# Kernel optimization log

Measured on AMD Instinct MI355X. Metric: run time of the kernel, lower is better.

The kernel has to match this reference:

```python
import jax, jax.numpy as jnp
import numpy as np

EMBED = 1024
HEADS = 16
HEAD_DIM = EMBED // HEADS
B, S = 2, 2048


def setup_inputs() -> dict:
    key = jax.random.key(0)
    ks = jax.random.split(key, 13)
    def lin(kw, kb):
        # torch nn.Linear default init: U(-1/sqrt(fan_in), 1/sqrt(fan_in))
        bound = 1.0 / np.sqrt(EMBED)
        W = jax.random.uniform(kw, (EMBED, EMBED), jnp.float32, -bound, bound)
        b = jax.random.uniform(kb, (EMBED,), jnp.float32, -bound, bound)
        return W, b
    Wq, bq = lin(ks[0], ks[1])
    Wk, bk = lin(ks[2], ks[3])
    Wv, bv = lin(ks[4], ks[5])
    Wo, bo = lin(ks[6], ks[7])
    return {
        "query": jax.random.normal(ks[8], (B, S, EMBED), jnp.float32),
        "key": jax.random.normal(ks[9], (B, S, EMBED), jnp.float32),
        "value": jax.random.normal(ks[10], (B, S, EMBED), jnp.float32),
        "mask": jax.random.randint(ks[11], (B, S, S), 0, 2, jnp.int32),
        "Wq": Wq, "bq": bq, "Wk": Wk, "bk": bk,
        "Wv": Wv, "bv": bv, "Wo": Wo, "bo": bo,
    }


def _split_heads(x):
    b, s, _ = x.shape
    return x.reshape(b, s, HEADS, HEAD_DIM).transpose(0, 2, 1, 3)  # [B,H,S,D]


def reference(query, key, value, mask, Wq, bq, Wk, bk, Wv, bv, Wo, bo):
    scaling = HEAD_DIM ** -0.5
    q = _split_heads(query @ Wq.T + bq) * scaling          # [B,H,Sq,D]
    k = _split_heads(key @ Wk.T + bk)                       # [B,H,Sk,D]
    v = _split_heads(value @ Wv.T + bv)                     # [B,H,Sk,D]
    scores = jnp.einsum('bhqd,bhkd->bhqk', q, k)            # [B,H,Sq,Sk]
    scores = jnp.where(mask[:, None, :, :] == 0, jnp.float32(-10000.0), scores)
    p = jax.nn.softmax(scores, axis=-1)
    x = jnp.einsum('bhqk,bhkd->bhqd', p, v)                 # [B,H,Sq,D]
    b, h, s, d = x.shape
    x = x.transpose(0, 2, 1, 3).reshape(b, s, h * d)
    return x @ Wo.T + bo
```

## Files before the change

kernel.cpp:

```cpp
#include <hip/hip_runtime.h>

#define EMBED 1024
#define HEADS 16
#define HDIM  64
#define BATCH 2
#define SEQ   2048
#define MTOT  (BATCH*SEQ)
#define LOG2E 1.4426950408889634f
#define QSCALE (0.125f * LOG2E)

typedef __attribute__((ext_vector_type(8)))  short short8;
typedef __attribute__((ext_vector_type(4)))  float f32x4;
typedef __attribute__((ext_vector_type(16))) float f32x16;

#define MFMA(a,b,c)   __builtin_amdgcn_mfma_f32_16x16x32_bf16(a,b,c,0,0,0)
#define MFMA32(a,b,c) __builtin_amdgcn_mfma_f32_32x32x16_bf16(a,b,c,0,0,0)

__device__ __forceinline__ ushort f2bf(float f) {
  union { float f; unsigned u; } v; v.f = f;
  unsigned u = v.u;
  unsigned r = u + 0x7fffu + ((u >> 16) & 1u);
  return (ushort)(r >> 16);
}
__device__ __forceinline__ unsigned packbf(float a, float b) {
  return (unsigned)f2bf(a) | ((unsigned)f2bf(b) << 16);
}
__device__ __forceinline__ unsigned cvtpk(float lo, float hi) {
  unsigned r;
  asm("v_cvt_pk_bf16_f32 %0, %1, %2" : "=v"(r) : "v"(lo), "v"(hi));
  return r;
}
__device__ __forceinline__ uint2 cvt4(float4 v) {
  uint2 r;
  asm("v_cvt_pk_bf16_f32 %0, %2, %3\n\t"
      "v_cvt_pk_bf16_f32 %1, %4, %5"
      : "=&v"(r.x), "=&v"(r.y)
      : "v"(v.x), "v"(v.y), "v"(v.z), "v"(v.w));
  return r;
}
__device__ __forceinline__ void gl_lds16(const ushort* g, ushort* l) {
  __builtin_amdgcn_global_load_lds(
      (const __attribute__((address_space(1))) unsigned*)g,
      (__attribute__((address_space(3))) unsigned*)l, 16, 0, 0);
}

__global__ __launch_bounds__(256) void tobf16(
    const float* __restrict__ s0, const float* __restrict__ s1, const float* __restrict__ s2,
    const float* __restrict__ s3, const float* __restrict__ s4, const float* __restrict__ s5,
    const float* __restrict__ s6,
    ushort* __restrict__ d0, ushort* __restrict__ d1, ushort* __restrict__ d2,
    ushort* __restrict__ d3, ushort* __restrict__ d4, ushort* __restrict__ d5,
    ushort* __restrict__ d6)
{
  const int z = blockIdx.z;
  const float* s; ushort* d;
  switch (z) {
    case 0: s = s0; d = d0; break;
    case 1: s = s1; d = d1; break;
    case 2: s = s2; d = d2; break;
    case 3: s = s3; d = d3; break;
    case 4: s = s4; d = d4; break;
    case 5: s = s5; d = d5; break;
    default: s = s6; d = d6; break;
  }
  const int nch = (z < 3) ? (MTOT * EMBED / 8) : (EMBED * EMBED / 8);
  int i = blockIdx.x * 256 + threadIdx.x;
  if (i >= nch) return;
  float4 a = reinterpret_cast<const float4*>(s)[2 * i];
  float4 b = reinterpret_cast<const float4*>(s)[2 * i + 1];
  uint2 lo = cvt4(a), hi = cvt4(b);
  reinterpret_cast<uint4*>(d)[i] = make_uint4(lo.x, lo.y, hi.x, hi.y);
}

__global__ __launch_bounds__(256) void maskpack(const int* __restrict__ mask,
                                                unsigned long long* __restrict__ bits) {
  size_t idx = (size_t)blockIdx.x * 256 + threadIdx.x;
  unsigned long long bal = __ballot(mask[idx] != 0);
  if ((threadIdx.x & 63) == 0) bits[idx >> 6] = bal;
}

template<int OM>
__global__ __launch_bounds__(256) void gemm_bf(
    const ushort* __restrict__ A0, const ushort* __restrict__ A1, const ushort* __restrict__ A2,
    const ushort* __restrict__ W0, const ushort* __restrict__ W1, const ushort* __restrict__ W2,
    const float* __restrict__ b0, const float* __restrict__ b1, const float* __restrict__ b2,
    ushort* __restrict__ oq, ushort* __restrict__ ok, ushort* __restrict__ ov,
    float* __restrict__ of)
{
  __shared__ __align__(16) ushort lds[2][2][4096];

  const int nwg = (OM == 0) ? 768 : 256;
  int lin = blockIdx.x + (blockIdx.y << 3);
  int swz = (lin & 7) * (nwg >> 3) + (lin >> 3);
  const int z  = swz >> 8;
  const int r_ = swz & 255;
  const int n0 = (r_ & 7) << 7;
  const int m0 = (r_ >> 3) << 7;

  const ushort* __restrict__ A    = (z == 0) ? A0 : (z == 1) ? A1 : A2;
  const ushort* __restrict__ W    = (z == 0) ? W0 : (z == 1) ? W1 : W2;
  const float*  __restrict__ bias = (z == 0) ? b0 : (z == 1) ? b1 : b2;

  const int t = threadIdx.x;
  const int lane = t & 63;
  const int wid = t >> 6;
  const int wr = wid >> 1, wc = wid & 1;
  const int lr = lane & 15, qg = lane >> 4;

  auto stage = [&](int buf, int k0) {
    #pragma unroll
    for (int it = 0; it < 2; ++it) {
      int idx = it * 256 + t;
      int row = idx >> 2;
      int col = ((idx & 3) ^ (row & 3)) << 3;
      gl_lds16(&A[(size_t)(m0 + row) * EMBED + k0 + col], &lds[buf][0][idx * 8]);
    }
    #pragma unroll
    for (int it = 0; it < 2; ++it) {
      int idx = it * 256 + t;
      int row = idx >> 2;
      int col = ((idx & 3) ^ (row & 3)) << 3;
      gl_lds16(&W[(size_t)(n0 + row) * EMBED + k0 + col], &lds[buf][1][idx * 8]);
    }
  };

  f32x4 acc[4][4] = {};

  stage(0, 0);
  asm volatile("s_waitcnt vmcnt(0)" ::: "memory");
  __syncthreads();

  for (int kt = 0; kt < EMBED / 32; ++kt) {
    const int buf = kt & 1;
    if (kt < EMBED / 32 - 1) stage(buf ^ 1, (kt + 1) * 32);

    short8 af[4], bfr[4];
    #pragma unroll
    for (int mi = 0; mi < 4; ++mi) {
      int row = wr * 64 + mi * 16 + lr;
      af[mi] = *reinterpret_cast<const short8*>(
          &lds[buf][0][row * 32 + ((qg ^ (row & 3)) << 3)]);
    }
    #pragma unroll
    for (int ni = 0; ni < 4; ++ni) {
      int row = wc * 64 + ni * 16 + lr;
      bfr[ni] = *reinterpret_cast<const short8*>(
          &lds[buf][1][row * 32 + ((qg ^ (row & 3)) << 3)]);
    }
    __builtin_amdgcn_s_setprio(1);
    #pragma unroll
    for (int mi = 0; mi < 4; ++mi)
      #pragma unroll
      for (int ni = 0; ni < 4; ++ni)
        acc[mi][ni] = MFMA(af[mi], bfr[ni], acc[mi][ni]);
    __builtin_amdgcn_s_setprio(0);
    __syncthreads();
  }

  #pragma unroll
  for (int ni = 0; ni < 4; ++ni) {
    int ng = n0 + wc * 64 + ni * 16 + lr;
    float bv_ = bias[ng];
    int h = ng >> 6, d = ng & 63;
    #pragma unroll
    for (int mi = 0; mi < 4; ++mi) {
      #pragma unroll
      for (int r = 0; r < 4; ++r) {
        int mg = m0 + wr * 64 + mi * 16 + qg * 4 + r;
        float val = acc[mi][ni][r] + bv_;
        if (OM == 1) {
          of[(size_t)mg * EMBED + ng] = val;
        } else {
          int bb = mg >> 11, s = mg & (SEQ - 1);
          int bh = bb * HEADS + h;
          if (z == 0)
            oq[((size_t)bh * SEQ + s) * HDIM + d] = f2bf(val * QSCALE);
          else if (z == 1)
            ok[((size_t)bh * SEQ + s) * HDIM + d] = f2bf(val);
          else {
            size_t addr = (((size_t)bh * 2 + (d >> 5)) * (SEQ / 32) + (s >> 5)) * 1024
                        + (size_t)(d & 31) * 32 + (s & 31);
            ov[addr] = f2bf(val);
          }
        }
      }
    }
  }
}

__global__ __launch_bounds__(256, 2) void attn(
    const ushort* __restrict__ qws, const ushort* __restrict__ kws,
    const ushort* __restrict__ vws, const unsigned* __restrict__ mbits,
    ushort* __restrict__ xws)
{
  const int t = threadIdx.x;
  const int wid = t >> 6;
  const int l = t & 63;
  const int q31 = l & 31;
  const int h = l >> 5;

  const int L = blockIdx.x;
  const int j = L >> 3;
  const int bh = ((L & 7) << 2) + (j >> 4);
  const int q0 = (j & 15) << 7;
  const int b = bh >> 4, head = bh & 15;

  __shared__ __align__(16) ushort lds[9216];

  const int qrow = q0 + wid * 32 + q31;
  const ushort* qp = qws + ((size_t)bh * SEQ + qrow) * HDIM + 8 * h;
  short8 qf[4];
  #pragma unroll
  for (int s = 0; s < 4; ++s)
    qf[s] = *reinterpret_cast<const short8*>(qp + 16 * s);

  const int rp = (q31 & 19) | ((q31 & 4) << 1) | ((q31 & 8) >> 1);

  int koff[4];
  #pragma unroll
  for (int i = 0; i < 4; ++i)
    koff[i] = rp * 64 + (((h + 2 * i) ^ (rp & 7)) << 3);
  int voff[2][2];
  #pragma unroll
  for (int sb = 0; sb < 2; ++sb)
    #pragma unroll
    for (int jj = 0; jj < 2; ++jj)
      voff[sb][jj] = sb * 1024 + q31 * 32 + (((h + 2 * jj) ^ (q31 & 3)) << 3);

  const ushort* ksb = kws + (size_t)bh * SEQ * HDIM
                    + ((t >> 3) << 6) + (((t & 7) ^ ((t >> 3) & 7)) << 3);
  const int vsub = t >> 7, vd = (t >> 2) & 31, vc = t & 3;
  const ushort* vsb = vws + (((size_t)bh * 2 + vsub) << 16)
                    + vd * 32 + ((vc ^ (vd & 3)) << 3);
  ushort* kd0 = lds + t * 8;
  ushort* vd0 = lds + 2048 + t * 8;

  const unsigned* mp = mbits + (size_t)(b * SEQ + qrow) * (SEQ / 32);

  f32x16 accT[2] = {};
  float ls0 = 0.f, ls1 = 0.f, ls2 = 0.f, ls3 = 0.f;

  auto STAGE = [&](int tile, int bb) {
    gl_lds16(ksb + (size_t)tile * 2048, kd0 + bb);
    gl_lds16(vsb + (size_t)tile * 1024, vd0 + bb);
  };

  auto COMP = [&](int bb, unsigned mwc) {
    const ushort* kb = lds + bb;
    const ushort* vb = lds + bb + 2048;
    short8 kf0 = *reinterpret_cast<const short8*>(kb + koff[0]);
    short8 kf1 = *reinterpret_cast<const short8*>(kb + koff[1]);
    short8 kf2 = *reinterpret_cast<const short8*>(kb + koff[2]);
    short8 kf3 = *reinterpret_cast<const short8*>(kb + koff[3]);
    __builtin_amdgcn_s_setprio(1);
    f32x16 s = {};
    s = MFMA32(kf0, qf[0], s);
    s = MFMA32(kf1, qf[1], s);
    s = MFMA32(kf2, qf[2], s);
    s = MFMA32(kf3, qf[3], s);
    __builtin_amdgcn_s_setprio(0);

    short8 vf0 = *reinterpret_cast<const short8*>(vb + voff[0][0]);
    short8 vf1 = *reinterpret_cast<const short8*>(vb + voff[0][1]);
    short8 vf2 = *reinterpret_cast<const short8*>(vb + voff[1][0]);
    short8 vf3 = *reinterpret_cast<const short8*>(vb + voff[1][1]);

    unsigned msh = mwc >> (8 * h);
    union U { unsigned u[4]; short8 s8; } p0u, p1u;
    #pragma unroll
    for (int i = 0; i < 8; ++i) {
      const int r0 = 2 * i, r1 = 2 * i + 1;
      float e0 = ((msh >> ((r0 & 7) + 16 * (r0 >> 3))) & 1u) ? __builtin_amdgcn_exp2f(s[r0]) : 0.0f;
      float e1 = ((msh >> ((r1 & 7) + 16 * (r1 >> 3))) & 1u) ? __builtin_amdgcn_exp2f(s[r1]) : 0.0f;
      if ((i & 3) == 0) ls0 += e0 + e1;
      else if ((i & 3) == 1) ls1 += e0 + e1;
      else if ((i & 3) == 2) ls2 += e0 + e1;
      else ls3 += e0 + e1;
      if (i < 4) p0u.u[i] = cvtpk(e0, e1);
      else       p1u.u[i - 4] = cvtpk(e0, e1);
    }

    __builtin_amdgcn_s_setprio(1);
    accT[0] = MFMA32(vf0, p0u.s8, accT[0]);
    accT[0] = MFMA32(vf1, p1u.s8, accT[0]);
    accT[1] = MFMA32(vf2, p0u.s8, accT[1]);
    accT[1] = MFMA32(vf3, p1u.s8, accT[1]);
    __builtin_amdgcn_s_setprio(0);
  };

  unsigned mw = *mp; ++mp;
  STAGE(0, 0);
  asm volatile("s_waitcnt vmcnt(0)" ::: "memory");
  __syncthreads();

  #pragma unroll 1
  for (int it = 0; it < 32; ++it) {
    STAGE(2 * it + 1, 4096);
    unsigned mn = *mp; ++mp;
    COMP(0, mw);
    asm volatile("s_waitcnt vmcnt(0)" ::: "memory");
    __syncthreads();
    mw = mn;
    if (it < 31) STAGE(2 * it + 2, 0);
    mn = *mp; ++mp;
    COMP(4096, mw);
    asm volatile("s_waitcnt vmcnt(0)" ::: "memory");
    __syncthreads();
    mw = mn;
  }

  float lsum = (ls0 + ls1) + (ls2 + ls3);
  float lrow = lsum + __shfl_xor(lsum, 32);
  float inv = 1.0f / lrow;

  ushort* xb = lds + wid * 2304;
  #pragma unroll
  for (int nb = 0; nb < 2; ++nb)
    #pragma unroll
    for (int rg = 0; rg < 4; ++rg) {
      int dbase = 32 * nb + 8 * rg + 4 * h;
      uint2 pk = make_uint2(
          packbf(accT[nb][4 * rg] * inv,     accT[nb][4 * rg + 1] * inv),
          packbf(accT[nb][4 * rg + 2] * inv, accT[nb][4 * rg + 3] * inv));
      *reinterpret_cast<uint2*>(&xb[q31 * 72 + dbase]) = pk;
    }
  asm volatile("" ::: "memory");
  #pragma unroll
  for (int pp = 0; pp < 4; ++pp) {
    int row = pp * 8 + (l >> 3);
    int col = (l & 7) * 8;
    short8 xv = *reinterpret_cast<const short8*>(&xb[row * 72 + col]);
    *reinterpret_cast<short8*>(
        &xws[((size_t)b * SEQ + q0 + wid * 32 + row) * EMBED + head * HDIM + col]) = xv;
  }
}

extern "C" void kernel_launch(void* const* d_in, const int* in_sizes, int n_in,
                              void* d_out, int out_size, void* d_ws, size_t ws_size,
                              hipStream_t stream) {
  (void)in_sizes; (void)n_in; (void)out_size; (void)ws_size;
  const float* query = (const float*)d_in[0];
  const float* key   = (const float*)d_in[1];
  const float* value = (const float*)d_in[2];
  const int*   mask  = (const int*)d_in[3];
  const float* Wq = (const float*)d_in[4];  const float* bq = (const float*)d_in[5];
  const float* Wk = (const float*)d_in[6];  const float* bk = (const float*)d_in[7];
  const float* Wv = (const float*)d_in[8];  const float* bv = (const float*)d_in[9];
  const float* Wo = (const float*)d_in[10]; const float* bo = (const float*)d_in[11];
  float* out = (float*)d_out;

  const size_t NQKV = (size_t)BATCH * HEADS * SEQ * HDIM;
  const size_t NW   = (size_t)EMBED * EMBED;
  ushort* qws = (ushort*)d_ws;
  ushort* kws = qws + NQKV;
  ushort* vws = kws + NQKV;
  ushort* xws = vws + NQKV;
  unsigned* mbits = (unsigned*)(xws + NQKV);
  ushort* aqb = (ushort*)(mbits + (size_t)BATCH * SEQ * SEQ / 32);
  ushort* akb = aqb + NQKV;
  ushort* avb = akb + NQKV;
  ushort* wqb = avb + NQKV;
  ushort* wkb = wqb + NW;
  ushort* wvb = wkb + NW;
  ushort* wob = wvb + NW;

  tobf16<<<dim3((NQKV / 8 + 255) / 256, 1, 7), 256, 0, stream>>>(
      query, key, value, Wq, Wk, Wv, Wo, aqb, akb, avb, wqb, wkb, wvb, wob);

  maskpack<<<(BATCH * SEQ * SEQ) / 256, 256, 0, stream>>>(mask, (unsigned long long*)mbits);

  gemm_bf<0><<<dim3(8, 96), 256, 0, stream>>>(
      aqb, akb, avb, wqb, wkb, wvb, bq, bk, bv, qws, kws, vws, nullptr);

  attn<<<dim3(512), 256, 0, stream>>>(qws, kws, vws, mbits, xws);

  gemm_bf<1><<<dim3(8, 32), 256, 0, stream>>>(
      xws, xws, xws, wob, wob, wob, bo, bo, bo, qws, kws, vws, out);
}
```

Measured before the change: 159.4 us.

## Triple-buffer GEMM LDS staging with partial vmcnt waits

Changes the projection GEMM's LDS staging from double to triple buffering. Two k-tiles are prefetched ahead, and each barrier waits only for the oldest outstanding loads (vmcnt(4)) rather than draining all global-to-LDS traffic. The goal is to hide global load latency behind MFMA work. LDS use grows from 32KB to 48KB per block, which may reduce occupancy, and correctness now depends on hand-counted vmcnt values.

```diff
diff --git a/kernel.cpp b/kernel.cpp
--- a/kernel.cpp
+++ b/kernel.cpp
@@ -87,7 +87,7 @@
     ushort* __restrict__ oq, ushort* __restrict__ ok, ushort* __restrict__ ov,
     float* __restrict__ of)
 {
-  __shared__ __align__(16) ushort lds[2][2][4096];
+  __shared__ __align__(16) ushort lds[3 * 8192];
 
   const int nwg = (OM == 0) ? 768 : 256;
   int lin = blockIdx.x + (blockIdx.y << 3);
@@ -108,44 +108,46 @@
   const int lr = lane & 15, qg = lane >> 4;
 
   auto stage = [&](int buf, int k0) {
+    ushort* dst = lds + buf * 8192;
     #pragma unroll
     for (int it = 0; it < 2; ++it) {
       int idx = it * 256 + t;
       int row = idx >> 2;
       int col = ((idx & 3) ^ (row & 3)) << 3;
-      gl_lds16(&A[(size_t)(m0 + row) * EMBED + k0 + col], &lds[buf][0][idx * 8]);
+      gl_lds16(&A[(size_t)(m0 + row) * EMBED + k0 + col], dst + idx * 8);
     }
     #pragma unroll
     for (int it = 0; it < 2; ++it) {
       int idx = it * 256 + t;
       int row = idx >> 2;
       int col = ((idx & 3) ^ (row & 3)) << 3;
-      gl_lds16(&W[(size_t)(n0 + row) * EMBED + k0 + col], &lds[buf][1][idx * 8]);
+      gl_lds16(&W[(size_t)(n0 + row) * EMBED + k0 + col], dst + 4096 + idx * 8);
     }
   };
 
   f32x4 acc[4][4] = {};
 
   stage(0, 0);
-  asm volatile("s_waitcnt vmcnt(0)" ::: "memory");
-  __syncthreads();
-
-  for (int kt = 0; kt < EMBED / 32; ++kt) {
-    const int buf = kt & 1;
-    if (kt < EMBED / 32 - 1) stage(buf ^ 1, (kt + 1) * 32);
-
+  stage(1, 32);
+  asm volatile("s_waitcnt vmcnt(4)" ::: "memory");
+  __builtin_amdgcn_s_barrier();
+  asm volatile("" ::: "memory");
+
+  for (int kt = 0; kt < 32; ++kt) {
+    const int buf = kt % 3;
+    if (kt < 30) stage((kt + 2) % 3, (kt + 2) * 32);
+
+    const ushort* ab = lds + buf * 8192;
     short8 af[4], bfr[4];
     #pragma unroll
     for (int mi = 0; mi < 4; ++mi) {
       int row = wr * 64 + mi * 16 + lr;
-      af[mi] = *reinterpret_cast<const short8*>(
-          &lds[buf][0][row * 32 + ((qg ^ (row & 3)) << 3)]);
+      af[mi] = *reinterpret_cast<const short8*>(ab + row * 32 + ((qg ^ (row & 3)) << 3));
     }
     #pragma unroll
     for (int ni = 0; ni < 4; ++ni) {
       int row = wc * 64 + ni * 16 + lr;
-      bfr[ni] = *reinterpret_cast<const short8*>(
-          &lds[buf][1][row * 32 + ((qg ^ (row & 3)) << 3)]);
+      bfr[ni] = *reinterpret_cast<const short8*>(ab + 4096 + row * 32 + ((qg ^ (row & 3)) << 3));
     }
     __builtin_amdgcn_s_setprio(1);
     #pragma unroll
@@ -154,7 +156,13 @@
       for (int ni = 0; ni < 4; ++ni)
         acc[mi][ni] = MFMA(af[mi], bfr[ni], acc[mi][ni]);
     __builtin_amdgcn_s_setprio(0);
-    __syncthreads();
+
+    if (kt < 30)       asm volatile("s_waitcnt vmcnt(4)" ::: "memory");
+    else if (kt == 30) asm volatile("s_waitcnt vmcnt(0)" ::: "memory");
+    if (kt < 31) {
+      __builtin_amdgcn_s_barrier();
+      asm volatile("" ::: "memory");
+    }
   }
 
   #pragma unroll
```

New measurement: 154.0 us. 1.04x faster.
